# Performance work log

Measured on AMD Instinct MI355X. Metric: run time of the kernel, lower is better.

Reference implementation:

```python
import jax, jax.numpy as jnp
import numpy as np

D_STATE = 16
D_CONV = 4


def silu(x):
    return x * jax.nn.sigmoid(x)


def selective_scan(x, dt, A, Bm, Cm, Dp):
    # x, dt: (B,L,P); A: (P,N); Bm, Cm: (B,L,N); Dp: (P,)
    dA = jnp.exp(dt[..., None] * A)                    # (B,L,P,N)
    dBx = (dt * x)[..., None] * Bm[:, :, None, :]      # (B,L,P,N)

    def comb(c1, c2):
        a1, b1 = c1
        a2, b2 = c2
        return a1 * a2, a2 * b1 + b2

    _, h = jax.lax.associative_scan(comb, (dA, dBx), axis=1)
    y = jnp.einsum('blpn,bln->blp', h, Cm) + x * Dp
    return y


def mamba(seq, W_in, conv_w, conv_b, W_x, W_dt, b_dt, A_log, Dp, W_out):
    # seq: (B, L, D_model)
    xz = seq @ W_in.T                                  # (B,L,2P)
    P = xz.shape[-1] // 2
    x, z = xz[..., :P], xz[..., P:]
    # causal depthwise conv over L
    xc = jnp.transpose(x, (0, 2, 1))                   # (B,P,L)
    xc = jax.lax.conv_general_dilated(xc, conv_w[:, None, :], (1,),
                                      [(D_CONV - 1, 0)], feature_group_count=P)
    x = silu(jnp.transpose(xc, (0, 2, 1)) + conv_b)    # (B,L,P)
    proj = x @ W_x.T                                   # (B,L, dt_rank+2N)
    dtr = W_dt.shape[1]
    dt = jax.nn.softplus(proj[..., :dtr] @ W_dt.T + b_dt)
    Bm = proj[..., dtr:dtr + D_STATE]
    Cm = proj[..., dtr + D_STATE:]
    A = -jnp.exp(A_log)
    y = selective_scan(x, dt, A, Bm, Cm, Dp)
    y = y * silu(z)
    return y @ W_out.T                                 # (B,L,D_model)


def oss_forward(x1, x2, W_in, conv_w, conv_b, W_x, W_dt, b_dt, A_log, Dp, W_out):
    B, C, H, W = x1.shape
    L = H * W
    seq_h = jnp.transpose(x1.reshape(B, C, L), (0, 2, 1))                       # (B, H*W, C) row-major
    seq_w = jnp.transpose(jnp.transpose(x1, (0, 1, 3, 2)).reshape(B, C, L), (0, 2, 1))  # column-major

    def run(i, s):
        return mamba(s, W_in[i], conv_w[i], conv_b[i], W_x[i], W_dt[i],
                     b_dt[i], A_log[i], Dp[i], W_out[i])

    y_hf = run(0, seq_h)
    y_hb = jnp.flip(run(1, jnp.flip(seq_h, 1)), 1)
    y_wf = run(2, seq_w)
    y_wb = jnp.flip(run(3, jnp.flip(seq_w, 1)), 1)

    y_h = jnp.transpose((y_hf + y_hb).reshape(B, H, W, C), (0, 3, 1, 2))        # (B,C,H,W)
    y_w = jnp.transpose((y_wf + y_wb).reshape(B, W, H, C), (0, 3, 2, 1))        # (B,C,H,W)
    return y_h + y_w + x2


def setup_inputs() -> dict:
    key = jax.random.key(0)
    ks = jax.random.split(key, 12)
    B, C, H, W = 2, 96, 64, 64
    P = 2 * C            # d_inner = expand * d_model = 192
    N = D_STATE
    dtr = -(-C // 16)    # dt_rank = ceil(C/16) = 6
    s = 0.02
    inp = {
        'x1': jax.random.normal(ks[0], (B, C, H, W), jnp.float32),
        'x2': jax.random.normal(ks[1], (B, C, H, W), jnp.float32),
        'W_in': jax.random.normal(ks[2], (4, 2 * P, C), jnp.float32) * s,
        'conv_w': jax.random.normal(ks[3], (4, P, D_CONV), jnp.float32) * s,
        'conv_b': jnp.zeros((4, P), jnp.float32),
        'W_x': jax.random.normal(ks[4], (4, dtr + 2 * N, P), jnp.float32) * s,
        'W_dt': jax.random.normal(ks[5], (4, P, dtr), jnp.float32) * s,
        'b_dt': jax.random.normal(ks[6], (4, P), jnp.float32) * s,
        'A_log': jnp.log(jnp.tile(jnp.arange(1.0, N + 1.0, dtype=jnp.float32), (4, P, 1))),
        'Dp': jnp.ones((4, P), jnp.float32),
        'W_out': jax.random.normal(ks[7], (4, C, P), jnp.float32) * s,
    }
    return inp


def reference(x1, x2, W_in, conv_w, conv_b, W_x, W_dt, b_dt, A_log, Dp, W_out):
    return oss_forward(x1, x2, W_in, conv_w, conv_b, W_x, W_dt, b_dt, A_log, Dp, W_out)
```

## Files before the change

kernel.cpp:

```cpp
#include <hip/hip_runtime.h>

#define D_DIRS 4
#define BB 2
#define CC 96
#define LL 4096
#define PP 192
#define TWOP 384
#define NN 16
#define DTR 6
#define NPROJ 38
#define NCH 256
#define CLEN 16
#define SEQT 24576
#define LOG2E 1.44269504088896340736f

typedef __bf16 bf16x8 __attribute__((ext_vector_type(8)));
typedef float f32x4 __attribute__((ext_vector_type(4)));

__device__ __forceinline__ float fast_softplus(float v) {
    return fmaxf(v, 0.0f) + __logf(1.0f + __expf(-fabsf(v)));
}

__device__ __constant__ float LOGN[16] = {
    0.0f, 0.6931471806f, 1.0986122887f, 1.3862943611f,
    1.6094379124f, 1.7917594692f, 1.9459101091f, 2.0794415417f,
    2.1972245773f, 2.3025850930f, 2.3978952728f, 2.4849066498f,
    2.5649493575f, 2.6390573296f, 2.7080502011f, 2.7725887222f };

#define POWERS(e1, E)                                                    \
    float E##2 = (e1)*(e1), E##4 = E##2*E##2, E##8 = E##4*E##4;          \
    float E##3 = E##2*(e1), E##5 = E##4*(e1), E##6 = E##4*E##2,          \
          E##7 = E##4*E##3, E##9 = E##8*(e1), E##10 = E##8*E##2,         \
          E##11 = E##8*E##3, E##12 = E##8*E##4, E##13 = E##8*E##5,       \
          E##14 = E##8*E##6, E##15 = E##8*E##7, E##16 = E##8*E##8;

__global__ void k_prep(const float* __restrict__ W_in, const float* __restrict__ W_x,
                       const float* __restrict__ W_out, __bf16* __restrict__ wbin,
                       __bf16* __restrict__ wbx, __bf16* __restrict__ wbout)
{
    int i = blockIdx.x * 256 + threadIdx.x;
    const int n0 = 4 * 384 * 104, n1 = 4 * 48 * 200, n2 = 4 * 96 * 200;
    if (i < n0) {
        int c = i % 104, jd = i / 104;
        wbin[i] = (c < 96) ? (__bf16)W_in[jd * 96 + c] : (__bf16)0.0f;
    } else if (i < n0 + n1) {
        int k = i - n0;
        int c = k % 200, jd = k / 200;
        int d = jd / 48, j = jd - d * 48;
        float v = (j < 38 && c < 192) ? W_x[(d * 38 + j) * 192 + c] : 0.0f;
        wbx[k] = (__bf16)v;
    } else if (i < n0 + n1 + n2) {
        int k = i - n0 - n1;
        int c = k % 200, jd = k / 200;
        float v = (c < 192) ? W_out[jd * 192 + c] : 0.0f;
        wbout[k] = (__bf16)v;
    }
}

__global__ __launch_bounds__(256) void k_img(
    const float* __restrict__ x1, __bf16* __restrict__ imgH, __bf16* __restrict__ imgW)
{
    __shared__ float t[96 * 65];
    const int b = blockIdx.y;
    const int lt = blockIdx.x;
    const int tid = threadIdx.x;
    for (int i = tid; i < 96 * 64; i += 256) {
        int c = i >> 6, lw = i & 63;
        t[c * 65 + lw] = x1[((b * 96 + c) << 12) + (lt << 6) + lw];
    }
    __syncthreads();
    for (int i = tid; i < 64 * 12; i += 256) {
        int lw = i / 12, q = i - lw * 12;
        union { __bf16 h[8]; uint4 u; } pk;
#pragma unroll
        for (int j = 0; j < 8; ++j) pk.h[j] = (__bf16)t[(q * 8 + j) * 65 + lw];
        ((uint4*)(imgH + (long)((b << 12) + (lt << 6) + lw) * 104))[q] = pk.u;
        ((uint4*)(imgW + (long)((b << 12) + (lw << 6) + lt) * 104))[q] = pk.u;
    }
}

__global__ __launch_bounds__(256) void k_gemm_in(
    const __bf16* __restrict__ imgH, const __bf16* __restrict__ imgW,
    const __bf16* __restrict__ wbin, float* __restrict__ xz_x, __bf16* __restrict__ zb)
{
    __shared__ __align__(16) __bf16 As[64 * 104];
    __shared__ __align__(16) __bf16 Bs[64 * 104];
    const int db = blockIdx.y;
    const int d = db >> 1, b = db & 1;
    const int t0 = blockIdx.x * 64;
    const int tid = threadIdx.x;
    const __bf16* img = (d < 2 ? imgH : imgW) + (long)b * (LL * 104);

    {
        uint4* adst = (uint4*)As;
        for (int i = tid; i < 832; i += 256) {
            int r = i / 13, q = i - r * 13;
            int l = (d & 1) ? (LL - 1 - (t0 + r)) : (t0 + r);
            adst[i] = ((const uint4*)(img + (long)l * 104))[q];
        }
    }

    const int lane = tid & 63;
    const int w = tid >> 6;
    const int wm = (w >> 1) * 32, wn = (w & 1) * 32;
    const int lr = lane & 15, lk = (lane >> 4) * 8;
    const int orow = (lane >> 4) * 4;

    for (int j0 = 0; j0 < TWOP; j0 += 64) {
        __syncthreads();
        {
            const uint4* bsrc = (const uint4*)(wbin + (long)(d * TWOP + j0) * 104);
            uint4* bdst = (uint4*)Bs;
            for (int i = tid; i < 832; i += 256) bdst[i] = bsrc[i];
        }
        __syncthreads();

        f32x4 acc[2][2] = {{{0.f,0.f,0.f,0.f},{0.f,0.f,0.f,0.f}},
                           {{0.f,0.f,0.f,0.f},{0.f,0.f,0.f,0.f}}};
#pragma unroll
        for (int ks = 0; ks < 96; ks += 32) {
            bf16x8 a0 = *(const bf16x8*)&As[(wm + lr) * 104 + ks + lk];
            bf16x8 a1 = *(const bf16x8*)&As[(wm + 16 + lr) * 104 + ks + lk];
            bf16x8 b0 = *(const bf16x8*)&Bs[(wn + lr) * 104 + ks + lk];
            bf16x8 b1 = *(const bf16x8*)&Bs[(wn + 16 + lr) * 104 + ks + lk];
            acc[0][0] = __builtin_amdgcn_mfma_f32_16x16x32_bf16(a0, b0, acc[0][0], 0, 0, 0);
            acc[0][1] = __builtin_amdgcn_mfma_f32_16x16x32_bf16(a0, b1, acc[0][1], 0, 0, 0);
            acc[1][0] = __builtin_amdgcn_mfma_f32_16x16x32_bf16(a1, b0, acc[1][0], 0, 0, 0);
            acc[1][1] = __builtin_amdgcn_mfma_f32_16x16x32_bf16(a1, b1, acc[1][1], 0, 0, 0);
        }
#pragma unroll
        for (int mi = 0; mi < 2; ++mi)
#pragma unroll
            for (int ni = 0; ni < 2; ++ni) {
                long mbase = (long)(db * LL + t0 + wm + mi * 16 + orow);
                int jcol = j0 + wn + ni * 16 + lr;
                if (j0 < PP) {
#pragma unroll
                    for (int r = 0; r < 4; ++r) xz_x[(mbase + r) * PP + jcol] = acc[mi][ni][r];
                } else {
#pragma unroll
                    for (int r = 0; r < 4; ++r) zb[(mbase + r) * PP + jcol - PP] = (__bf16)acc[mi][ni][r];
                }
            }
    }
}

__global__ __launch_bounds__(192) void k_conv(
    const float* __restrict__ xz_x, const float* __restrict__ conv_w,
    const float* __restrict__ conv_b, __bf16* __restrict__ xb16)
{
    __shared__ float xs[67 * 192];
    const int db = blockIdx.y;
    const int t0 = blockIdx.x * 64;
    const int d = db >> 1;
    const int m0 = db * LL + t0;
    const int tid = threadIdx.x;

    const float4* src = (const float4*)(xz_x + ((long)m0 - 3) * PP);
    for (int i = tid; i < 67 * 48; i += 192) {
        float4 v;
        if (t0 == 0 && i < 144) v = make_float4(0.f, 0.f, 0.f, 0.f);
        else v = src[i];
        ((float4*)xs)[i] = v;
    }

    const int p = tid;
    const float* wp = conv_w + (d * PP + p) * 4;
    float w0 = wp[0], w1 = wp[1], w2 = wp[2], w3 = wp[3];
    float bias = conv_b[d * PP + p];
    __syncthreads();

    for (int t = 0; t < 64; ++t) {
        float acc = bias + w0 * xs[t * PP + p] + w1 * xs[(t + 1) * PP + p]
                         + w2 * xs[(t + 2) * PP + p] + w3 * xs[(t + 3) * PP + p];
        float s = acc / (1.0f + __expf(-acc));
        xb16[(long)(m0 + t) * 200 + p] = (__bf16)s;
    }
}

__global__ __launch_bounds__(256) void k_gemm_proj(
    const __bf16* __restrict__ xb16, const __bf16* __restrict__ wbx, float* __restrict__ proj)
{
    __shared__ __align__(16) __bf16 As[64 * 200];
    __shared__ __align__(16) __bf16 Bs[48 * 200];
    const int m0 = blockIdx.x * 64;
    const int d = m0 >> 13;
    const int tid = threadIdx.x;

    for (int i = tid; i < 1600; i += 256) {
        int r = i / 25, q = i - r * 25;
        ((uint4*)As)[i] = ((const uint4*)(xb16 + (long)(m0 + r) * 200))[q];
    }
    {
        const uint4* bsrc = (const uint4*)(wbx + (long)d * 48 * 200);
        uint4* bdst = (uint4*)Bs;
        for (int i = tid; i < 1200; i += 256) bdst[i] = bsrc[i];
    }
    __syncthreads();

    const int lane = tid & 63;
    const int w = tid >> 6;
    const int lr = lane & 15, lk = (lane >> 4) * 8;
    const int orow = (lane >> 4) * 4;

    f32x4 acc[3] = {{0.f,0.f,0.f,0.f},{0.f,0.f,0.f,0.f},{0.f,0.f,0.f,0.f}};
#pragma unroll
    for (int ks = 0; ks < 192; ks += 32) {
        bf16x8 a = *(const bf16x8*)&As[(w * 16 + lr) * 200 + ks + lk];
#pragma unroll
        for (int ni = 0; ni < 3; ++ni) {
            bf16x8 bfr = *(const bf16x8*)&Bs[(ni * 16 + lr) * 200 + ks + lk];
            acc[ni] = __builtin_amdgcn_mfma_f32_16x16x32_bf16(a, bfr, acc[ni], 0, 0, 0);
        }
    }
#pragma unroll
    for (int ni = 0; ni < 3; ++ni) {
        int j = ni * 16 + lr;
        if (j < NPROJ) {
#pragma unroll
            for (int r = 0; r < 4; ++r) {
                int m = m0 + w * 16 + orow + r;
                proj[(long)m * NPROJ + j] = acc[ni][r];
            }
        }
    }
}

__global__ __launch_bounds__(256) void k_gemm_out(
    const __bf16* __restrict__ ysb, const __bf16* __restrict__ wbout, float* __restrict__ yo)
{
    __shared__ __align__(16) __bf16 As[64 * 200];
    __shared__ __align__(16) __bf16 Bs[96 * 200];
    const int m0 = blockIdx.x * 64;
    const int d = m0 >> 13;
    const int tid = threadIdx.x;

    for (int i = tid; i < 1600; i += 256) {
        int r = i / 25, q = i - r * 25;
        ((uint4*)As)[i] = ((const uint4*)(ysb + (long)(m0 + r) * 200))[q];
    }
    {
        const uint4* bsrc = (const uint4*)(wbout + (long)d * 96 * 200);
        uint4* bdst = (uint4*)Bs;
        for (int i = tid; i < 2400; i += 256) bdst[i] = bsrc[i];
    }
    __syncthreads();

    const int lane = tid & 63;
    const int w = tid >> 6;
    const int wm = (w >> 1) * 32, wn = (w & 1) * 48;
    const int lr = lane & 15, lk = (lane >> 4) * 8;
    const int orow = (lane >> 4) * 4;

    f32x4 acc[2][3] = {};
#pragma unroll
    for (int ks = 0; ks < 192; ks += 32) {
        bf16x8 a0 = *(const bf16x8*)&As[(wm + lr) * 200 + ks + lk];
        bf16x8 a1 = *(const bf16x8*)&As[(wm + 16 + lr) * 200 + ks + lk];
#pragma unroll
        for (int ni = 0; ni < 3; ++ni) {
            bf16x8 bfr = *(const bf16x8*)&Bs[(wn + ni * 16 + lr) * 200 + ks + lk];
            acc[0][ni] = __builtin_amdgcn_mfma_f32_16x16x32_bf16(a0, bfr, acc[0][ni], 0, 0, 0);
            acc[1][ni] = __builtin_amdgcn_mfma_f32_16x16x32_bf16(a1, bfr, acc[1][ni], 0, 0, 0);
        }
    }
#pragma unroll
    for (int mi = 0; mi < 2; ++mi)
#pragma unroll
        for (int ni = 0; ni < 3; ++ni) {
#pragma unroll
            for (int r = 0; r < 4; ++r) {
                int m = m0 + wm + mi * 16 + orow + r;
                yo[(long)m * CC + wn + ni * 16 + lr] = acc[mi][ni][r];
            }
        }
}

__global__ __launch_bounds__(384) void k_pass1(
    const __bf16* __restrict__ xb16, const float* __restrict__ proj,
    const float* __restrict__ A_log, const float* __restrict__ W_dt,
    const float* __restrict__ b_dt,
    float* __restrict__ cb_pa, float* __restrict__ cb_h)
{
    __shared__ __align__(16) float pl[2][CLEN * 40];
    __shared__ __align__(16) __bf16 xsb[2][CLEN * 200];
    const int tid = threadIdx.x;
    const int sub = tid / 192;
    const int p = tid - sub * 192;
    const int chunk = blockIdx.x * 2 + sub;
    const int db = blockIdx.y;
    const int d = db >> 1;
    const int m0 = db * LL + chunk * CLEN;

    const float* pr = proj + (long)m0 * NPROJ;
    for (int i = p; i < CLEN * NPROJ; i += 192) {
        int r = i / NPROJ, c = i - r * NPROJ;
        int col = (c < 6) ? c : c + 2;
        pl[sub][r * 40 + col] = pr[i];
    }
    for (int i = p; i < 400; i += 192) {
        int r = i / 25, q = i - r * 25;
        ((uint4*)xsb[sub])[i] = ((const uint4*)(xb16 + (long)(m0 + r) * 200))[q];
    }

    bool fastA = true;
    float A2[16];
    {
        const float* al = A_log + (d * PP + p) * NN;
#pragma unroll
        for (int n = 0; n < 16; ++n) {
            float av = al[n];
            fastA = fastA && (fabsf(av - LOGN[n]) < 1e-4f);
            A2[n] = av;
        }
    }
    float w[6];
    const float* wd = W_dt + (d * PP + p) * DTR;
#pragma unroll
    for (int r = 0; r < 6; ++r) w[r] = wd[r];
    const float bdt = b_dt[d * PP + p];
    float h[16];
#pragma unroll
    for (int n = 0; n < 16; ++n) h[n] = 0.f;
    float sdt = 0.f;
    __syncthreads();

    if (fastA) {
#pragma unroll
        for (int s = 0; s < CLEN; ++s) {
            const float* row = pl[sub] + s * 40;
            float4 d0 = *(const float4*)(row);
            float4 d1 = *(const float4*)(row + 4);
            float v = bdt + d0.x*w[0] + d0.y*w[1] + d0.z*w[2] + d0.w*w[3] + d1.x*w[4] + d1.y*w[5];
            float dtv = fast_softplus(v);
            sdt += dtv;
            float dtx = dtv * (float)xsb[sub][s * 200 + p];
            float e1 = exp2f(-LOG2E * dtv);
            POWERS(e1, e)
            const float4* B4 = (const float4*)(row + 8);
            float4 B0 = B4[0], B1 = B4[1], B2v = B4[2], B3 = B4[3];
            h[0]  = e1 *h[0]  + dtx*B0.x;  h[1]  = e2 *h[1]  + dtx*B0.y;
            h[2]  = e3 *h[2]  + dtx*B0.z;  h[3]  = e4 *h[3]  + dtx*B0.w;
            h[4]  = e5 *h[4]  + dtx*B1.x;  h[5]  = e6 *h[5]  + dtx*B1.y;
            h[6]  = e7 *h[6]  + dtx*B1.z;  h[7]  = e8 *h[7]  + dtx*B1.w;
            h[8]  = e9 *h[8]  + dtx*B2v.x; h[9]  = e10*h[9]  + dtx*B2v.y;
            h[10] = e11*h[10] + dtx*B2v.z; h[11] = e12*h[11] + dtx*B2v.w;
            h[12] = e13*h[12] + dtx*B3.x;  h[13] = e14*h[13] + dtx*B3.y;
            h[14] = e15*h[14] + dtx*B3.z;  h[15] = e16*h[15] + dtx*B3.w;
        }
        const long cbase = (long)chunk * SEQT + db * PP + p;
        float pe1 = exp2f(-LOG2E * sdt);
        POWERS(pe1, pe)
        float pa[16] = {pe1,pe2,pe3,pe4,pe5,pe6,pe7,pe8,pe9,pe10,pe11,pe12,pe13,pe14,pe15,pe16};
#pragma unroll
        for (int n = 0; n < 16; ++n) {
            cb_pa[cbase + n * 1536] = pa[n];
            cb_h [cbase + n * 1536] = h[n];
        }
    } else {
#pragma unroll
        for (int n = 0; n < 16; ++n) A2[n] = -__expf(A2[n]) * LOG2E;
        for (int s = 0; s < CLEN; ++s) {
            const float* row = pl[sub] + s * 40;
            float4 d0 = *(const float4*)(row);
            float4 d1 = *(const float4*)(row + 4);
            float v = bdt + d0.x*w[0] + d0.y*w[1] + d0.z*w[2] + d0.w*w[3] + d1.x*w[4] + d1.y*w[5];
            float dtv = fast_softplus(v);
            sdt += dtv;
            float dtx = dtv * (float)xsb[sub][s * 200 + p];
            const float* B = row + 8;
#pragma unroll
            for (int n = 0; n < 16; ++n)
                h[n] = exp2f(dtv * A2[n]) * h[n] + dtx * B[n];
        }
        const long cbase = (long)chunk * SEQT + db * PP + p;
#pragma unroll
        for (int n = 0; n < 16; ++n) {
            cb_pa[cbase + n * 1536] = exp2f(A2[n] * sdt);
            cb_h [cbase + n * 1536] = h[n];
        }
    }
}

__global__ void k_chunkscan(const float* __restrict__ cb_pa, float* __restrict__ cb_h)
{
    int j = blockIdx.x * 256 + threadIdx.x;
    float run = 0.0f;
    for (int c = 0; c < NCH; c += 8) {
        float pa[8], hh[8];
#pragma unroll
        for (int i = 0; i < 8; ++i) {
            long o = (long)(c + i) * SEQT + j;
            pa[i] = cb_pa[o]; hh[i] = cb_h[o];
        }
#pragma unroll
        for (int i = 0; i < 8; ++i) {
            cb_h[(long)(c + i) * SEQT + j] = run;
            run = pa[i] * run + hh[i];
        }
    }
}

__global__ __launch_bounds__(384) void k_pass2(
    const __bf16* __restrict__ xb16, const float* __restrict__ proj,
    const float* __restrict__ A_log, const float* __restrict__ W_dt,
    const float* __restrict__ b_dt, const float* __restrict__ Dp,
    const __bf16* __restrict__ zb, const float* __restrict__ cb_h,
    __bf16* __restrict__ ysb)
{
    __shared__ __align__(16) float pl[2][CLEN * 40];
    __shared__ __align__(16) __bf16 xsb[2][CLEN * 200];
    __shared__ __align__(16) __bf16 zs[2][CLEN * PP];
    const int tid = threadIdx.x;
    const int sub = tid / 192;
    const int p = tid - sub * 192;
    const int chunk = blockIdx.x * 2 + sub;
    const int db = blockIdx.y;
    const int d = db >> 1;
    const int m0 = db * LL + chunk * CLEN;

    const float* pr = proj + (long)m0 * NPROJ;
    for (int i = p; i < CLEN * NPROJ; i += 192) {
        int r = i / NPROJ, c = i - r * NPROJ;
        int col = (c < 6) ? c : c + 2;
        pl[sub][r * 40 + col] = pr[i];
    }
    for (int i = p; i < 400; i += 192) {
        int r = i / 25, q = i - r * 25;
        ((uint4*)xsb[sub])[i] = ((const uint4*)(xb16 + (long)(m0 + r) * 200))[q];
    }
    {
        const uint4* zsrc = (const uint4*)(zb + (long)m0 * PP);
        ((uint4*)zs[sub])[p] = zsrc[p];
        ((uint4*)zs[sub])[p + 192] = zsrc[p + 192];
    }

    bool fastA = true;
    float A2[16];
    {
        const float* al = A_log + (d * PP + p) * NN;
#pragma unroll
        for (int n = 0; n < 16; ++n) {
            float av = al[n];
            fastA = fastA && (fabsf(av - LOGN[n]) < 1e-4f);
            A2[n] = av;
        }
    }
    float w[6];
    const float* wd = W_dt + (d * PP + p) * DTR;
#pragma unroll
    for (int r = 0; r < 6; ++r) w[r] = wd[r];
    const float bdt = b_dt[d * PP + p];
    const float Dv = Dp[d * PP + p];

    float h[16];
    const long cbase = (long)chunk * SEQT + db * PP + p;
#pragma unroll
    for (int n = 0; n < 16; ++n) h[n] = cb_h[cbase + n * 1536];
    __syncthreads();

    if (fastA) {
#pragma unroll
        for (int s = 0; s < CLEN; ++s) {
            const float* row = pl[sub] + s * 40;
            float4 d0 = *(const float4*)(row);
            float4 d1 = *(const float4*)(row + 4);
            float v = bdt + d0.x*w[0] + d0.y*w[1] + d0.z*w[2] + d0.w*w[3] + d1.x*w[4] + d1.y*w[5];
            float dtv = fast_softplus(v);
            float xvv = (float)xsb[sub][s * 200 + p];
            float dtx = dtv * xvv;
            float e1 = exp2f(-LOG2E * dtv);
            POWERS(e1, e)
            const float4* B4 = (const float4*)(row + 8);
            const float4* C4 = (const float4*)(row + 24);
            float4 B0 = B4[0], B1 = B4[1], B2v = B4[2], B3 = B4[3];
            float4 C0 = C4[0], C1 = C4[1], C2v = C4[2], C3 = C4[3];
            float y = 0.f;
            h[0]  = e1 *h[0]  + dtx*B0.x;  y += h[0] *C0.x;
            h[1]  = e2 *h[1]  + dtx*B0.y;  y += h[1] *C0.y;
            h[2]  = e3 *h[2]  + dtx*B0.z;  y += h[2] *C0.z;
            h[3]  = e4 *h[3]  + dtx*B0.w;  y += h[3] *C0.w;
            h[4]  = e5 *h[4]  + dtx*B1.x;  y += h[4] *C1.x;
            h[5]  = e6 *h[5]  + dtx*B1.y;  y += h[5] *C1.y;
            h[6]  = e7 *h[6]  + dtx*B1.z;  y += h[6] *C1.z;
            h[7]  = e8 *h[7]  + dtx*B1.w;  y += h[7] *C1.w;
            h[8]  = e9 *h[8]  + dtx*B2v.x; y += h[8] *C2v.x;
            h[9]  = e10*h[9]  + dtx*B2v.y; y += h[9] *C2v.y;
            h[10] = e11*h[10] + dtx*B2v.z; y += h[10]*C2v.z;
            h[11] = e12*h[11] + dtx*B2v.w; y += h[11]*C2v.w;
            h[12] = e13*h[12] + dtx*B3.x;  y += h[12]*C3.x;
            h[13] = e14*h[13] + dtx*B3.y;  y += h[13]*C3.y;
            h[14] = e15*h[14] + dtx*B3.z;  y += h[14]*C3.z;
            h[15] = e16*h[15] + dtx*B3.w;  y += h[15]*C3.w;
            float zvv = (float)zs[sub][s * PP + p];
            ysb[(long)(m0 + s) * 200 + p] = (__bf16)((y + xvv * Dv) * (zvv / (1.0f + __expf(-zvv))));
        }
    } else {
#pragma unroll
        for (int n = 0; n < 16; ++n) A2[n] = -__expf(A2[n]) * LOG2E;
        for (int s = 0; s < CLEN; ++s) {
            const float* row = pl[sub] + s * 40;
            float4 d0 = *(const float4*)(row);
            float4 d1 = *(const float4*)(row + 4);
            float v = bdt + d0.x*w[0] + d0.y*w[1] + d0.z*w[2] + d0.w*w[3] + d1.x*w[4] + d1.y*w[5];
            float dtv = fast_softplus(v);
            float xvv = (float)xsb[sub][s * 200 + p];
            float dtx = dtv * xvv;
            const float* B = row + 8;
            const float* C = row + 24;
            float y = 0.f;
#pragma unroll
            for (int n = 0; n < 16; ++n) {
                h[n] = exp2f(dtv * A2[n]) * h[n] + dtx * B[n];
                y += h[n] * C[n];
            }
            float zvv = (float)zs[sub][s * PP + p];
            ysb[(long)(m0 + s) * 200 + p] = (__bf16)((y + xvv * Dv) * (zvv / (1.0f + __expf(-zvv))));
        }
    }
}

__global__ void k_final(const float* __restrict__ x2, const float* __restrict__ yo,
                        float* __restrict__ out)
{
    int idx = blockIdx.x * blockDim.x + threadIdx.x;
    const int total = BB * CC * LL;
    for (; idx < total; idx += gridDim.x * blockDim.x) {
        int w = idx & 63;
        int h = (idx >> 6) & 63;
        int c = (idx >> 12) % CC;
        int b = idx / (CC * LL);
        int lh = (h << 6) | w;
        int lw = (w << 6) | h;
        long m0 = (long)(0 * BB + b) * LL + lh;
        long m1 = (long)(1 * BB + b) * LL + (LL - 1 - lh);
        long m2 = (long)(2 * BB + b) * LL + lw;
        long m3 = (long)(3 * BB + b) * LL + (LL - 1 - lw);
        out[idx] = x2[idx] + yo[m0 * CC + c] + yo[m1 * CC + c] + yo[m2 * CC + c] + yo[m3 * CC + c];
    }
}

extern "C" void kernel_launch(void* const* d_in, const int* in_sizes, int n_in,
                              void* d_out, int out_size, void* d_ws, size_t ws_size,
                              hipStream_t stream)
{
    const float* x1     = (const float*)d_in[0];
    const float* x2     = (const float*)d_in[1];
    const float* W_in   = (const float*)d_in[2];
    const float* conv_w = (const float*)d_in[3];
    const float* conv_b = (const float*)d_in[4];
    const float* W_x    = (const float*)d_in[5];
    const float* W_dt   = (const float*)d_in[6];
    const float* b_dt   = (const float*)d_in[7];
    const float* A_log  = (const float*)d_in[8];
    const float* Dp     = (const float*)d_in[9];
    const float* W_out  = (const float*)d_in[10];
    float* out = (float*)d_out;
    float* ws  = (float*)d_ws;

    float*  xz_x  = ws;
    __bf16* zb    = (__bf16*)(ws + 6291456);
    __bf16* xb16  = (__bf16*)(ws + 9437184);
    float*  proj  = ws + 12713984;
    float*  cb_pa = ws + 13959168;
    float*  cb_h  = ws + 20250624;
    __bf16* imgH  = (__bf16*)(ws + 26542080);
    __bf16* imgW  = (__bf16*)(ws + 26968064);
    __bf16* wbin  = (__bf16*)(ws + 27394048);
    __bf16* wbx   = (__bf16*)(ws + 27473920);
    __bf16* wbout = (__bf16*)(ws + 27493120);
    __bf16* ysb = (__bf16*)xz_x;
    float*  yo  = cb_pa;

    k_prep<<<dim3(1074), 256, 0, stream>>>(W_in, W_x, W_out, wbin, wbx, wbout);
    k_img<<<dim3(64, 2), 256, 0, stream>>>(x1, imgH, imgW);
    k_gemm_in<<<dim3(64, 8), 256, 0, stream>>>(imgH, imgW, wbin, xz_x, zb);
    k_conv<<<dim3(64, 8), 192, 0, stream>>>(xz_x, conv_w, conv_b, xb16);
    k_gemm_proj<<<dim3(512), 256, 0, stream>>>(xb16, wbx, proj);
    k_pass1<<<dim3(NCH / 2, 8), 384, 0, stream>>>(xb16, proj, A_log, W_dt, b_dt, cb_pa, cb_h);
    k_chunkscan<<<dim3(SEQT / 256), 256, 0, stream>>>(cb_pa, cb_h);
    k_pass2<<<dim3(NCH / 2, 8), 384, 0, stream>>>(xb16, proj, A_log, W_dt, b_dt, Dp, zb, cb_h, ysb);
    k_gemm_out<<<dim3(512), 256, 0, stream>>>(ysb, wbout, yo);
    k_final<<<dim3(3072), 256, 0, stream>>>(x2, yo, out);
}
```

Measured before the change: 151.8 us.

## Pad proj rows and read scan inputs directly from global instead of LDS staging

The projection GEMM now writes its output with a padded stride of 40 and the dt/B/C columns already realigned, so the scan kernels can do aligned float4 loads straight from global memory. Both scan passes drop their LDS staging of proj, x and z and the barrier that followed it. They now launch one 192-thread block per chunk instead of two chunks per 384-thread block. This aims to cut the staging copy and sync latency and raise occupancy, at the cost of redundant broadcast global/L1 loads of the per-row proj values across all 192 threads. Workspace offsets are shifted to make room for the padded proj buffer.

```diff
diff --git a/kernel.cpp b/kernel.cpp
--- a/kernel.cpp
+++ b/kernel.cpp
@@ -9,6 +9,7 @@
 #define NN 16
 #define DTR 6
 #define NPROJ 38
+#define PROJW 40
 #define NCH 256
 #define CLEN 16
 #define SEQT 24576
@@ -217,10 +218,11 @@
     for (int ni = 0; ni < 3; ++ni) {
         int j = ni * 16 + lr;
         if (j < NPROJ) {
+            int col = (j < 6) ? j : j + 2;
 #pragma unroll
             for (int r = 0; r < 4; ++r) {
                 int m = m0 + w * 16 + orow + r;
-                proj[(long)m * NPROJ + j] = acc[ni][r];
+                proj[(long)m * PROJW + col] = acc[ni][r];
             }
         }
     }
@@ -276,32 +278,17 @@
         }
 }
 
-__global__ __launch_bounds__(384) void k_pass1(
+__global__ __launch_bounds__(192) void k_pass1(
     const __bf16* __restrict__ xb16, const float* __restrict__ proj,
     const float* __restrict__ A_log, const float* __restrict__ W_dt,
     const float* __restrict__ b_dt,
     float* __restrict__ cb_pa, float* __restrict__ cb_h)
 {
-    __shared__ __align__(16) float pl[2][CLEN * 40];
-    __shared__ __align__(16) __bf16 xsb[2][CLEN * 200];
-    const int tid = threadIdx.x;
-    const int sub = tid / 192;
-    const int p = tid - sub * 192;
-    const int chunk = blockIdx.x * 2 + sub;
+    const int p = threadIdx.x;
+    const int chunk = blockIdx.x;
     const int db = blockIdx.y;
     const int d = db >> 1;
     const int m0 = db * LL + chunk * CLEN;
-
-    const float* pr = proj + (long)m0 * NPROJ;
-    for (int i = p; i < CLEN * NPROJ; i += 192) {
-        int r = i / NPROJ, c = i - r * NPROJ;
-        int col = (c < 6) ? c : c + 2;
-        pl[sub][r * 40 + col] = pr[i];
-    }
-    for (int i = p; i < 400; i += 192) {
-        int r = i / 25, q = i - r * 25;
-        ((uint4*)xsb[sub])[i] = ((const uint4*)(xb16 + (long)(m0 + r) * 200))[q];
-    }
 
     bool fastA = true;
     float A2[16];
@@ -323,18 +310,20 @@
 #pragma unroll
     for (int n = 0; n < 16; ++n) h[n] = 0.f;
     float sdt = 0.f;
-    __syncthreads();
+
+    const float* prow = proj + (long)m0 * PROJW;
+    const __bf16* xrow = xb16 + (long)m0 * 200 + p;
 
     if (fastA) {
 #pragma unroll
         for (int s = 0; s < CLEN; ++s) {
-            const float* row = pl[sub] + s * 40;
+            const float* row = prow + s * PROJW;
             float4 d0 = *(const float4*)(row);
             float4 d1 = *(const float4*)(row + 4);
             float v = bdt + d0.x*w[0] + d0.y*w[1] + d0.z*w[2] + d0.w*w[3] + d1.x*w[4] + d1.y*w[5];
             float dtv = fast_softplus(v);
             sdt += dtv;
-            float dtx = dtv * (float)xsb[sub][s * 200 + p];
+            float dtx = dtv * (float)xrow[s * 200];
             float e1 = exp2f(-LOG2E * dtv);
             POWERS(e1, e)
             const float4* B4 = (const float4*)(row + 8);
@@ -361,13 +350,13 @@
 #pragma unroll
         for (int n = 0; n < 16; ++n) A2[n] = -__expf(A2[n]) * LOG2E;
         for (int s = 0; s < CLEN; ++s) {
-            const float* row = pl[sub] + s * 40;
+            const float* row = prow + s * PROJW;
             float4 d0 = *(const float4*)(row);
             float4 d1 = *(const float4*)(row + 4);
             float v = bdt + d0.x*w[0] + d0.y*w[1] + d0.z*w[2] + d0.w*w[3] + d1.x*w[4] + d1.y*w[5];
             float dtv = fast_softplus(v);
             sdt += dtv;
-            float dtx = dtv * (float)xsb[sub][s * 200 + p];
+            float dtx = dtv * (float)xrow[s * 200];
             const float* B = row + 8;
 #pragma unroll
             for (int n = 0; n < 16; ++n)
@@ -401,39 +390,18 @@
     }
 }
 
-__global__ __launch_bounds__(384) void k_pass2(
+__global__ __launch_bounds__(192) void k_pass2(
     const __bf16* __restrict__ xb16, const float* __restrict__ proj,
     const float* __restrict__ A_log, const float* __restrict__ W_dt,
     const float* __restrict__ b_dt, const float* __restrict__ Dp,
     const __bf16* __restrict__ zb, const float* __restrict__ cb_h,
     __bf16* __restrict__ ysb)
 {
-    __shared__ __align__(16) float pl[2][CLEN * 40];
-    __shared__ __align__(16) __bf16 xsb[2][CLEN * 200];
-    __shared__ __align__(16) __bf16 zs[2][CLEN * PP];
-    const int tid = threadIdx.x;
-    const int sub = tid / 192;
-    const int p = tid - sub * 192;
-    const int chunk = blockIdx.x * 2 + sub;
+    const int p = threadIdx.x;
+    const int chunk = blockIdx.x;
     const int db = blockIdx.y;
     const int d = db >> 1;
     const int m0 = db * LL + chunk * CLEN;
-
-    const float* pr = proj + (long)m0 * NPROJ;
-    for (int i = p; i < CLEN * NPROJ; i += 192) {
-        int r = i / NPROJ, c = i - r * NPROJ;
-        int col = (c < 6) ? c : c + 2;
-        pl[sub][r * 40 + col] = pr[i];
-    }
-    for (int i = p; i < 400; i += 192) {
-        int r = i / 25, q = i - r * 25;
-        ((uint4*)xsb[sub])[i] = ((const uint4*)(xb16 + (long)(m0 + r) * 200))[q];
-    }
-    {
-        const uint4* zsrc = (const uint4*)(zb + (long)m0 * PP);
-        ((uint4*)zs[sub])[p] = zsrc[p];
-        ((uint4*)zs[sub])[p + 192] = zsrc[p + 192];
-    }
 
     bool fastA = true;
     float A2[16];
@@ -457,17 +425,21 @@
     const long cbase = (long)chunk * SEQT + db * PP + p;
 #pragma unroll
     for (int n = 0; n < 16; ++n) h[n] = cb_h[cbase + n * 1536];
-    __syncthreads();
+
+    const float* prow = proj + (long)m0 * PROJW;
+    const __bf16* xrow = xb16 + (long)m0 * 200 + p;
+    const __bf16* zrow = zb + (long)m0 * PP + p;
+    __bf16* yrow = ysb + (long)m0 * 200 + p;
 
     if (fastA) {
 #pragma unroll
         for (int s = 0; s < CLEN; ++s) {
-            const float* row = pl[sub] + s * 40;
+            const float* row = prow + s * PROJW;
             float4 d0 = *(const float4*)(row);
             float4 d1 = *(const float4*)(row + 4);
             float v = bdt + d0.x*w[0] + d0.y*w[1] + d0.z*w[2] + d0.w*w[3] + d1.x*w[4] + d1.y*w[5];
             float dtv = fast_softplus(v);
-            float xvv = (float)xsb[sub][s * 200 + p];
+            float xvv = (float)xrow[s * 200];
             float dtx = dtv * xvv;
             float e1 = exp2f(-LOG2E * dtv);
             POWERS(e1, e)
@@ -492,19 +464,19 @@
             h[13] = e14*h[13] + dtx*B3.y;  y += h[13]*C3.y;
             h[14] = e15*h[14] + dtx*B3.z;  y += h[14]*C3.z;
             h[15] = e16*h[15] + dtx*B3.w;  y += h[15]*C3.w;
-            float zvv = (float)zs[sub][s * PP + p];
-            ysb[(long)(m0 + s) * 200 + p] = (__bf16)((y + xvv * Dv) * (zvv / (1.0f + __expf(-zvv))));
+            float zvv = (float)zrow[s * PP];
+            yrow[s * 200] = (__bf16)((y + xvv * Dv) * (zvv / (1.0f + __expf(-zvv))));
         }
     } else {
 #pragma unroll
         for (int n = 0; n < 16; ++n) A2[n] = -__expf(A2[n]) * LOG2E;
         for (int s = 0; s < CLEN; ++s) {
-            const float* row = pl[sub] + s * 40;
+            const float* row = prow + s * PROJW;
             float4 d0 = *(const float4*)(row);
             float4 d1 = *(const float4*)(row + 4);
             float v = bdt + d0.x*w[0] + d0.y*w[1] + d0.z*w[2] + d0.w*w[3] + d1.x*w[4] + d1.y*w[5];
             float dtv = fast_softplus(v);
-            float xvv = (float)xsb[sub][s * 200 + p];
+            float xvv = (float)xrow[s * 200];
             float dtx = dtv * xvv;
             const float* B = row + 8;
             const float* C = row + 24;
@@ -514,8 +486,8 @@
                 h[n] = exp2f(dtv * A2[n]) * h[n] + dtx * B[n];
                 y += h[n] * C[n];
             }
-            float zvv = (float)zs[sub][s * PP + p];
-            ysb[(long)(m0 + s) * 200 + p] = (__bf16)((y + xvv * Dv) * (zvv / (1.0f + __expf(-zvv))));
+            float zvv = (float)zrow[s * PP];
+            yrow[s * 200] = (__bf16)((y + xvv * Dv) * (zvv / (1.0f + __expf(-zvv))));
         }
     }
 }
@@ -562,13 +534,13 @@
     __bf16* zb    = (__bf16*)(ws + 6291456);
     __bf16* xb16  = (__bf16*)(ws + 9437184);
     float*  proj  = ws + 12713984;
-    float*  cb_pa = ws + 13959168;
-    float*  cb_h  = ws + 20250624;
-    __bf16* imgH  = (__bf16*)(ws + 26542080);
-    __bf16* imgW  = (__bf16*)(ws + 26968064);
-    __bf16* wbin  = (__bf16*)(ws + 27394048);
-    __bf16* wbx   = (__bf16*)(ws + 27473920);
-    __bf16* wbout = (__bf16*)(ws + 27493120);
+    float*  cb_pa = ws + 14024704;
+    float*  cb_h  = ws + 20316160;
+    __bf16* imgH  = (__bf16*)(ws + 26607616);
+    __bf16* imgW  = (__bf16*)(ws + 27033600);
+    __bf16* wbin  = (__bf16*)(ws + 27459584);
+    __bf16* wbx   = (__bf16*)(ws + 27539456);
+    __bf16* wbout = (__bf16*)(ws + 27558656);
     __bf16* ysb = (__bf16*)xz_x;
     float*  yo  = cb_pa;
 
@@ -577,9 +549,9 @@
     k_gemm_in<<<dim3(64, 8), 256, 0, stream>>>(imgH, imgW, wbin, xz_x, zb);
     k_conv<<<dim3(64, 8), 192, 0, stream>>>(xz_x, conv_w, conv_b, xb16);
     k_gemm_proj<<<dim3(512), 256, 0, stream>>>(xb16, wbx, proj);
-    k_pass1<<<dim3(NCH / 2, 8), 384, 0, stream>>>(xb16, proj, A_log, W_dt, b_dt, cb_pa, cb_h);
+    k_pass1<<<dim3(NCH, 8), 192, 0, stream>>>(xb16, proj, A_log, W_dt, b_dt, cb_pa, cb_h);
     k_chunkscan<<<dim3(SEQT / 256), 256, 0, stream>>>(cb_pa, cb_h);
-    k_pass2<<<dim3(NCH / 2, 8), 384, 0, stream>>>(xb16, proj, A_log, W_dt, b_dt, Dp, zb, cb_h, ysb);
+    k_pass2<<<dim3(NCH, 8), 192, 0, stream>>>(xb16, proj, A_log, W_dt, b_dt, Dp, zb, cb_h, ysb);
     k_gemm_out<<<dim3(512), 256, 0, stream>>>(ysb, wbout, yo);
     k_final<<<dim3(3072), 256, 0, stream>>>(x2, yo, out);
 }
```

After: 145.5 us. 4.2% less time.
